# Optimization experiments

Hardware: AMD Instinct MI355X
Metric: run time of the kernel (lower is better)

## Reference

```python
import jax, jax.numpy as jnp
import numpy as np

EPS = 1e-5
NUM_HEADS = 16


def activation_quant(x):
    # 8-bit activation quant with straight-through estimator
    scale = 127.0 / jnp.clip(jnp.max(jnp.abs(x), axis=-1, keepdims=True), 1e-5, None)
    y = jnp.clip(jnp.round(x * scale), -128.0, 127.0) / scale
    return x + jax.lax.stop_gradient(y - x)


def weight_quant(w):
    # ternary {-1,0,1} weight quant with STE
    scale = 1.0 / jnp.clip(jnp.mean(jnp.abs(w)), 1e-5, None)
    wq = jnp.clip(jnp.round(w * scale), -1.0, 1.0) / scale
    return w + jax.lax.stop_gradient(wq - w)


def bitlinear(x, w):
    # F.layer_norm(x, x.shape[1:]): normalize over ALL dims except batch, no affine
    axes = tuple(range(1, x.ndim))
    mu = jnp.mean(x, axis=axes, keepdims=True)
    var = jnp.var(x, axis=axes, keepdims=True)
    xn = (x - mu) * jax.lax.rsqrt(var + EPS)
    return jnp.einsum('bnd,od->bno', activation_quant(xn), weight_quant(w))


def layer_norm(x, gamma, beta):
    mu = jnp.mean(x, axis=-1, keepdims=True)
    var = jnp.var(x, axis=-1, keepdims=True)
    return (x - mu) * jax.lax.rsqrt(var + EPS) * gamma + beta


def setup_inputs() -> dict:
    key = jax.random.key(0)
    k0, k1, k2 = jax.random.split(key, 3)
    B, N, D = 2, 2048, 1024
    return {
        't': jnp.zeros((1,), jnp.float32),
        'x': jax.random.normal(k0, (B, N, D), jnp.float32),
        'w_qkv': jax.random.normal(k1, (3 * D, D), jnp.float32) * 0.02,
        'w_out': jax.random.normal(k2, (D, D), jnp.float32) * 0.02,
        'gamma': jnp.ones((D,), jnp.float32),
        'beta': jnp.zeros((D,), jnp.float32),
    }


def reference(t, x, w_qkv, w_out, gamma, beta):
    B, N, D = x.shape
    H = NUM_HEADS
    hd = D // H
    scale = hd ** -0.5
    h = layer_norm(x, gamma, beta)                     # [B,N,D]
    qkv = bitlinear(h, w_qkv).reshape(B, N, 3, H, hd)   # [B,N,3,H,hd]
    qkv = jnp.transpose(qkv, (2, 0, 3, 1, 4))           # [3,B,H,N,hd]
    q, k, v = qkv[0], qkv[1], qkv[2]
    attn = jax.nn.softmax(jnp.einsum('bhnd,bhmd->bhnm', q, k) * scale, axis=-1)
    out = jnp.einsum('bhnm,bhmd->bhnd', attn, v)        # [B,H,N,hd]
    out = jnp.transpose(out, (0, 2, 1, 3)).reshape(B, N, D)
    return bitlinear(out, w_out)
```

## Files before the change

### kernel.cpp

```cpp
#include <hip/hip_runtime.h>
#include <hip/hip_bf16.h>
#include <hip/hip_fp16.h>
#include <math.h>

typedef __hip_bfloat16 bf16;
typedef int   i32x4 __attribute__((ext_vector_type(4)));
typedef float f32x4 __attribute__((ext_vector_type(4)));
typedef short bfx8  __attribute__((ext_vector_type(8)));

#define EPSV 1e-5f
#define NROWS 4096
#define DIM   1024
#define NSEQ  2048

__device__ __forceinline__ float ldv(const void* p, size_t i, int dt){
  if (dt == 0) return ((const float*)p)[i];
  if (dt == 1) return __bfloat162float(((const bf16*)p)[i]);
  return __half2float(((const __half*)p)[i]);
}

__device__ __forceinline__ void detect(const void* c0, const void* c1,
                                       int& dt, const void*& g, const void*& bta){
  unsigned u0 = *(const unsigned*)c0;
  int gfirst = (u0 != 0u) ? 1 : 0;
  g   = gfirst ? c0 : c1;
  bta = gfirst ? c1 : c0;
  unsigned short g0 = *(const unsigned short*)g;
  dt = (g0 == 0x3F80) ? 1 : ((g0 == 0x3C00) ? 2 : 0);
}

__device__ __forceinline__ float blk_sum(float v, float* sm){
  #pragma unroll
  for (int o = 32; o > 0; o >>= 1) v += __shfl_xor(v, o, 64);
  __syncthreads();
  if ((threadIdx.x & 63) == 0) sm[threadIdx.x >> 6] = v;
  __syncthreads();
  return sm[0] + sm[1] + sm[2] + sm[3];
}
__device__ __forceinline__ double blk_sum_d(double v, double* sm){
  #pragma unroll
  for (int o = 32; o > 0; o >>= 1) v += __shfl_xor(v, o, 64);
  __syncthreads();
  if ((threadIdx.x & 63) == 0) sm[threadIdx.x >> 6] = v;
  __syncthreads();
  return sm[0] + sm[1] + sm[2] + sm[3];
}
__device__ __forceinline__ float blk_max(float v, float* sm){
  #pragma unroll
  for (int o = 32; o > 0; o >>= 1) v = fmaxf(v, __shfl_xor(v, o, 64));
  __syncthreads();
  if ((threadIdx.x & 63) == 0) sm[threadIdx.x >> 6] = v;
  __syncthreads();
  return fmaxf(fmaxf(sm[0], sm[1]), fmaxf(sm[2], sm[3]));
}

__global__ __launch_bounds__(256) void ln_rows(const void* __restrict__ x,
                                               const void* __restrict__ c0,
                                               const void* __restrict__ c1,
                                               float* __restrict__ h,
                                               double* __restrict__ lnp){
  __shared__ float sm[4];
  __shared__ double smd[4];
  int dt; const void *g, *bta;
  detect(c0, c1, dt, g, bta);
  int row = blockIdx.x;
  int tid = threadIdx.x;
  float v[4]; float s = 0.f;
  float gmv[4], btv[4];
  if (dt == 0){
    float4 v4 = ((const float4*)x)[(size_t)row*256 + tid];
    v[0]=v4.x; v[1]=v4.y; v[2]=v4.z; v[3]=v4.w;
    float4 gm4 = ((const float4*)g)[tid];
    float4 bt4 = ((const float4*)bta)[tid];
    gmv[0]=gm4.x; gmv[1]=gm4.y; gmv[2]=gm4.z; gmv[3]=gm4.w;
    btv[0]=bt4.x; btv[1]=bt4.y; btv[2]=bt4.z; btv[3]=bt4.w;
  } else {
    size_t base = (size_t)row * DIM;
    #pragma unroll
    for (int i = 0; i < 4; ++i){
      v[i]   = ldv(x, base + 4*tid + i, dt);
      gmv[i] = ldv(g, 4*tid + i, dt);
      btv[i] = ldv(bta, 4*tid + i, dt);
    }
  }
  #pragma unroll
  for (int i = 0; i < 4; ++i) s += v[i];
  s = blk_sum(s, sm);
  float mu = s * (1.f/1024.f);
  float d2 = 0.f;
  #pragma unroll
  for (int i = 0; i < 4; ++i){ float d = v[i] - mu; d2 += d*d; }
  d2 = blk_sum(d2, sm);
  float rs = rsqrtf(d2 * (1.f/1024.f) + EPSV);
  float hv[4];
  #pragma unroll
  for (int i = 0; i < 4; ++i) hv[i] = (v[i]-mu)*rs*gmv[i] + btv[i];
  ((float4*)h)[(size_t)row*256 + tid] = make_float4(hv[0],hv[1],hv[2],hv[3]);
  double hs = 0.0, hq = 0.0;
  #pragma unroll
  for (int i = 0; i < 4; ++i){ hs += (double)hv[i]; hq += (double)hv[i]*(double)hv[i]; }
  hs = blk_sum_d(hs, smd);
  hq = blk_sum_d(hq, smd);
  if (tid == 0){ lnp[2*row] = hs; lnp[2*row + 1] = hq; }
}

__global__ __launch_bounds__(256) void abs_reduce_both(const void* __restrict__ wq,
                                                       const void* __restrict__ wo,
                                                       double* __restrict__ awp1,
                                                       double* __restrict__ awp2,
                                                       const void* __restrict__ c0,
                                                       const void* __restrict__ c1){
  __shared__ double smd[4];
  int dt; const void *g, *bta;
  detect(c0, c1, dt, g, bta);
  int blk = blockIdx.x;
  const void* w; int n; int nblk; int bi; double* part;
  if (blk < 512){ w = wq; n = 3*DIM*DIM; nblk = 512; bi = blk;      part = awp1; }
  else          { w = wo; n = DIM*DIM;   nblk = 128; bi = blk - 512; part = awp2; }
  double s = 0.0;
  if (dt == 0){
    const float4* w4 = (const float4*)w;
    int n4 = n >> 2;
    for (int i = bi*256 + threadIdx.x; i < n4; i += nblk*256){
      float4 v = w4[i];
      s += (double)(fabsf(v.x) + fabsf(v.y)) + (double)(fabsf(v.z) + fabsf(v.w));
    }
  } else {
    for (int i = bi*256 + threadIdx.x; i < n; i += nblk*256)
      s += (double)fabsf(ldv(w, i, dt));
  }
  s = blk_sum_d(s, smd);
  if (threadIdx.x == 0) part[bi] = s;
}

__global__ __launch_bounds__(256) void finalize1(float* acc,
                                                 const double* __restrict__ lnp,
                                                 const double* __restrict__ awp1,
                                                 const double* __restrict__ awp2){
  __shared__ double smd[4];
  int tid = threadIdx.x;
  double s0=0, q0=0, s1=0, q1=0, a1=0, a2=0;
  for (int i = tid; i < 2048; i += 256){
    s0 += lnp[2*i];          q0 += lnp[2*i + 1];
    s1 += lnp[2*(i+2048)];   q1 += lnp[2*(i+2048) + 1];
  }
  for (int i = tid; i < 512; i += 256) a1 += awp1[i];
  if (tid < 128) a2 = awp2[tid];
  s0 = blk_sum_d(s0, smd);  q0 = blk_sum_d(q0, smd);
  s1 = blk_sum_d(s1, smd);  q1 = blk_sum_d(q1, smd);
  a1 = blk_sum_d(a1, smd);  a2 = blk_sum_d(a2, smd);
  if (tid == 0){
    const double cnt = 2097152.0;
    double mu0 = s0/cnt, var0 = q0/cnt - mu0*mu0;
    double mu1 = s1/cnt, var1 = q1/cnt - mu1*mu1;
    acc[16] = (float)mu0; acc[17] = (float)(1.0 / sqrt(var0 + 1e-5));
    acc[18] = (float)mu1; acc[19] = (float)(1.0 / sqrt(var1 + 1e-5));
    acc[20] = (float)(1.0 / fmax(a1 / (3.0*1024.0*1024.0), 1e-5));
    acc[21] = (float)(1.0 / fmax(a2 / (1024.0*1024.0), 1e-5));
  }
}

__global__ __launch_bounds__(256) void finalize2(float* acc,
                                                 const double* __restrict__ atp){
  __shared__ double smd[4];
  int tid = threadIdx.x;
  double s0=0, q0=0, s1=0, q1=0;
  for (int i = tid; i < 512; i += 256){
    s0 += atp[2*i];          q0 += atp[2*i + 1];
    s1 += atp[2*(i+512)];    q1 += atp[2*(i+512) + 1];
  }
  s0 = blk_sum_d(s0, smd);  q0 = blk_sum_d(q0, smd);
  s1 = blk_sum_d(s1, smd);  q1 = blk_sum_d(q1, smd);
  if (tid == 0){
    const double cnt = 2097152.0;
    double mu0 = s0/cnt, var0 = q0/cnt - mu0*mu0;
    double mu1 = s1/cnt, var1 = q1/cnt - mu1*mu1;
    acc[22] = (float)mu0; acc[23] = (float)(1.0 / sqrt(var0 + 1e-5));
    acc[24] = (float)mu1; acc[25] = (float)(1.0 / sqrt(var1 + 1e-5));
  }
}

__global__ __launch_bounds__(256) void act_quant_i8(const float* __restrict__ buf,
                                                    signed char* __restrict__ qout,
                                                    float* __restrict__ rscale,
                                                    const float* __restrict__ acc,
                                                    int statOff){
  __shared__ float sm[4];
  int row = blockIdx.x;
  int b = row >> 11;
  float mu = acc[statOff + 2*b], rs = acc[statOff + 2*b + 1];
  int tid = threadIdx.x;
  float4 v4 = ((const float4*)buf)[(size_t)row*256 + tid];
  float v[4] = {(v4.x-mu)*rs, (v4.y-mu)*rs, (v4.z-mu)*rs, (v4.w-mu)*rs};
  float am = fmaxf(fmaxf(fabsf(v[0]), fabsf(v[1])), fmaxf(fabsf(v[2]), fabsf(v[3])));
  am = blk_max(am, sm);
  am = fmaxf(am, 1e-5f);
  float s127 = 127.f / am;
  unsigned pk = 0;
  #pragma unroll
  for (int i = 0; i < 4; ++i){
    float q = rintf(v[i] * s127);
    q = fminf(fmaxf(q, -128.f), 127.f);
    pk |= ((unsigned)(unsigned char)(signed char)q) << (8*i);
  }
  ((unsigned*)qout)[(size_t)row*256 + tid] = pk;
  if (tid == 0) rscale[row] = am * (1.f/127.f);
}

__global__ __launch_bounds__(256) void w_quant_both(const void* __restrict__ wqv,
                                                    const void* __restrict__ wov,
                                                    signed char* __restrict__ wqk,
                                                    signed char* __restrict__ wqo,
                                                    const float* __restrict__ acc,
                                                    const void* __restrict__ c0,
                                                    const void* __restrict__ c1){
  int dt; const void *g, *bta;
  detect(c0, c1, dt, g, bta);
  const int NQ4 = 786432;
  const int NT4 = 1048576;
  float s1 = acc[20], s2 = acc[21];
  if (dt == 0){
    for (int i = blockIdx.x*256 + threadIdx.x; i < NT4; i += gridDim.x*256){
      int inq = (i < NQ4);
      const float4* src = inq ? (const float4*)wqv : (const float4*)wov;
      unsigned* dst = inq ? (unsigned*)wqk : (unsigned*)wqo;
      int idx = inq ? i : (i - NQ4);
      float scale = inq ? s1 : s2;
      float4 v = src[idx];
      float vv[4] = {v.x, v.y, v.z, v.w};
      unsigned pk = 0;
      #pragma unroll
      for (int j = 0; j < 4; ++j){
        float q = rintf(vv[j] * scale);
        q = fminf(fmaxf(q, -1.f), 1.f);
        pk |= ((unsigned)(unsigned char)(signed char)q) << (8*j);
      }
      dst[idx] = pk;
    }
  } else {
    const int NQ = 3*DIM*DIM, NT = 4*DIM*DIM;
    for (int i = blockIdx.x*256 + threadIdx.x; i < NT; i += gridDim.x*256){
      int inq = (i < NQ);
      int idx = inq ? i : (i - NQ);
      float scale = inq ? s1 : s2;
      float q = rintf(ldv(inq ? wqv : wov, idx, dt) * scale);
      q = fminf(fmaxf(q, -1.f), 1.f);
      (inq ? wqk : wqo)[idx] = (signed char)q;
    }
  }
}

__global__ __launch_bounds__(256) void gemm_i8(const signed char* __restrict__ A,
                                               const signed char* __restrict__ W,
                                               const float* __restrict__ rscale,
                                               const float* __restrict__ acc, int sidx,
                                               float* __restrict__ Cf,
                                               bf16* __restrict__ Cb,
                                               int ldc, int writeBf, float q_prescale){
  __shared__ __attribute__((aligned(16))) signed char Asl[128][80];
  __shared__ __attribute__((aligned(16))) signed char Bsl[128][80];
  int tid = threadIdx.x, lane = tid & 63, w = tid >> 6;
  int wr = w >> 1, wc = w & 1;

  int nwgx = gridDim.x;
  int flat = blockIdx.y * nwgx + blockIdx.x;
  int nwg  = nwgx * gridDim.y;
  int cpx  = nwg >> 3;
  int swz  = (flat & 7) * cpx + (flat >> 3);
  int r0 = (swz / nwgx) * 128, o0 = (swz % nwgx) * 128;

  i32x4 zz = {0,0,0,0};
  i32x4 accv[4][4];
  #pragma unroll
  for (int m = 0; m < 4; ++m)
    #pragma unroll
    for (int n = 0; n < 4; ++n) accv[m][n] = zz;

  int sr0 = tid >> 2, sr1 = sr0 + 64;
  int sc  = (tid & 3) * 16;

  i32x4 a0, a1, b0, b1;
  a0 = *(const i32x4*)(A + (size_t)(r0 + sr0)*1024 + sc);
  a1 = *(const i32x4*)(A + (size_t)(r0 + sr1)*1024 + sc);
  b0 = *(const i32x4*)(W + (size_t)(o0 + sr0)*1024 + sc);
  b1 = *(const i32x4*)(W + (size_t)(o0 + sr1)*1024 + sc);

  for (int k0 = 0; k0 < 1024; k0 += 64){
    __syncthreads();
    *(i32x4*)&Asl[sr0][sc] = a0;
    *(i32x4*)&Asl[sr1][sc] = a1;
    *(i32x4*)&Bsl[sr0][sc] = b0;
    *(i32x4*)&Bsl[sr1][sc] = b1;
    __syncthreads();
    if (k0 + 64 < 1024){
      int kn = k0 + 64;
      a0 = *(const i32x4*)(A + (size_t)(r0 + sr0)*1024 + kn + sc);
      a1 = *(const i32x4*)(A + (size_t)(r0 + sr1)*1024 + kn + sc);
      b0 = *(const i32x4*)(W + (size_t)(o0 + sr0)*1024 + kn + sc);
      b1 = *(const i32x4*)(W + (size_t)(o0 + sr1)*1024 + kn + sc);
    }
    i32x4 af[4], bfr[4];
    #pragma unroll
    for (int m = 0; m < 4; ++m)
      af[m] = *(const i32x4*)&Asl[wr*64 + m*16 + (lane & 15)][(lane >> 4) * 16];
    #pragma unroll
    for (int n = 0; n < 4; ++n)
      bfr[n] = *(const i32x4*)&Bsl[wc*64 + n*16 + (lane & 15)][(lane >> 4) * 16];
    __builtin_amdgcn_s_setprio(1);
    #pragma unroll
    for (int m = 0; m < 4; ++m)
      #pragma unroll
      for (int n = 0; n < 4; ++n)
        accv[m][n] = __builtin_amdgcn_mfma_i32_16x16x64_i8(af[m], bfr[n], accv[m][n], 0, 0, 0);
    __builtin_amdgcn_s_setprio(0);
  }

  float wsc = acc[sidx];
  float cs = (o0 < 1024) ? q_prescale : 1.0f;
  float rf[4][4];
  #pragma unroll
  for (int m = 0; m < 4; ++m)
    #pragma unroll
    for (int r = 0; r < 4; ++r)
      rf[m][r] = rscale[r0 + wr*64 + m*16 + ((lane >> 4) << 2) + r] / wsc * cs;

  #pragma unroll
  for (int m = 0; m < 4; ++m)
    #pragma unroll
    for (int n = 0; n < 4; ++n)
      #pragma unroll
      for (int r = 0; r < 4; ++r){
        float val = (float)accv[m][n][r] * rf[m][r];
        size_t row = (size_t)(r0 + wr*64 + m*16 + ((lane >> 4) << 2) + r);
        int col = o0 + wc*64 + n*16 + (lane & 15);
        if (writeBf) Cb[row * ldc + col] = __float2bfloat16(val);
        else         Cf[row * ldc + col] = val;
      }
}

__global__ __launch_bounds__(256) void attn_mfma(const bf16* __restrict__ qkv,
                                                 float* __restrict__ out,
                                                 double* __restrict__ atp){
  __shared__ __attribute__((aligned(16))) unsigned short K_lds[64][64];
  __shared__ __attribute__((aligned(16))) unsigned short Vt_lds[64][64];
  __shared__ __attribute__((aligned(16))) unsigned short P_lds[4][16][64];
  __shared__ double smd[4];

  int tid = threadIdx.x, lane = tid & 63, w = tid >> 6;
  int l15 = lane & 15, g = lane >> 4;
  int h7 = l15 & 7;

  int flat = blockIdx.y * 32 + blockIdx.x;
  int slot = flat & 7, idx = flat >> 3;
  int bh = slot * 4 + (idx >> 5);
  int qx = idx & 31;
  int b = bh >> 4, h = bh & 15;
  int n0 = qx * 64;
  const unsigned short* qg = (const unsigned short*)qkv;

  char* kB = (char*)K_lds;
  char* vB = (char*)Vt_lds;
  char* pB = (char*)P_lds + w*2048;

  bfx8 qf[2];
  #pragma unroll
  for (int s = 0; s < 2; ++s){
    int qrow = b*NSEQ + n0 + w*16 + l15;
    qf[s] = *(const bfx8*)(qg + (size_t)qrow*3072 + h*64 + g*8 + s*32);
  }

  float m_run = -INFINITY, l_run = 0.f;
  f32x4 zf = {0.f, 0.f, 0.f, 0.f};
  f32x4 acco[4];
  #pragma unroll
  for (int n = 0; n < 4; ++n) acco[n] = zf;

  int krow = lane;
  int r2 = tid & 31, dwin = tid >> 5;
  int lh7 = lane & 7;

  bfx8 kc0, kc1, vv0, vv1;
  auto LOADT = [&](int kt){
    size_t kvb = (size_t)(b*NSEQ + kt*64);
    kc0 = *(const bfx8*)(qg + (kvb + krow)*3072 + 1024 + h*64 + w*8);
    kc1 = *(const bfx8*)(qg + (kvb + krow)*3072 + 1024 + h*64 + (w + 4)*8);
    vv0 = *(const bfx8*)(qg + (kvb + 2*r2    )*3072 + 2048 + h*64 + dwin*8);
    vv1 = *(const bfx8*)(qg + (kvb + 2*r2 + 1)*3072 + 2048 + h*64 + dwin*8);
  };
  LOADT(0);

  for (int kt = 0; kt < NSEQ/64; ++kt){
    __syncthreads();
    *(bfx8*)(kB + krow*128 + (((w    ) ^ lh7) << 4)) = kc0;
    *(bfx8*)(kB + krow*128 + (((w + 4) ^ lh7) << 4)) = kc1;
    #pragma unroll
    for (int u = 0; u < 8; ++u){
      unsigned word = (unsigned)(unsigned short)vv0[u] |
                      ((unsigned)(unsigned short)vv1[u] << 16);
      *(unsigned*)(vB + (dwin*8 + u)*128 + ((4*r2) ^ (u << 4))) = word;
    }
    __syncthreads();
    if (kt + 1 < NSEQ/64) LOADT(kt + 1);

    f32x4 sacc[4];
    #pragma unroll
    for (int f = 0; f < 4; ++f) sacc[f] = zf;
    #pragma unroll
    for (int f = 0; f < 4; ++f){
      bfx8 kb0 = *(const bfx8*)(kB + (f*16 + l15)*128 + (((g    ) ^ h7) << 4));
      bfx8 kb1 = *(const bfx8*)(kB + (f*16 + l15)*128 + (((g + 4) ^ h7) << 4));
      __builtin_amdgcn_s_setprio(1);
      sacc[f] = __builtin_amdgcn_mfma_f32_16x16x32_bf16(kb0, qf[0], sacc[f], 0, 0, 0);
      sacc[f] = __builtin_amdgcn_mfma_f32_16x16x32_bf16(kb1, qf[1], sacc[f], 0, 0, 0);
      __builtin_amdgcn_s_setprio(0);
    }

    float pm = sacc[0][0];
    #pragma unroll
    for (int f = 0; f < 4; ++f)
      #pragma unroll
      for (int r = 0; r < 4; ++r) pm = fmaxf(pm, sacc[f][r]);
    pm = fmaxf(pm, __shfl_xor(pm, 16, 64));
    pm = fmaxf(pm, __shfl_xor(pm, 32, 64));
    if (__any(pm > m_run + 8.f)){
      float mnew = fmaxf(m_run, pm);
      float corr = __expf(m_run - mnew);
      m_run = mnew;
      l_run *= corr;
      float ca[4];
      #pragma unroll
      for (int r = 0; r < 4; ++r) ca[r] = __shfl(corr, 4*g + r, 64);
      #pragma unroll
      for (int n = 0; n < 4; ++n)
        #pragma unroll
        for (int r = 0; r < 4; ++r) acco[n][r] *= ca[r];
    }
    float p[4][4]; float ts = 0.f;
    #pragma unroll
    for (int f = 0; f < 4; ++f)
      #pragma unroll
      for (int r = 0; r < 4; ++r){
        p[f][r] = __expf(sacc[f][r] - m_run);
        ts += p[f][r];
      }
    ts += __shfl_xor(ts, 16, 64);
    ts += __shfl_xor(ts, 32, 64);
    l_run += ts;

    #pragma unroll
    for (int f = 0; f < 4; ++f)
      #pragma unroll
      for (int rp = 0; rp < 2; ++rp){
        unsigned pk;
        asm("v_cvt_pk_bf16_f32 %0, %1, %2" : "=v"(pk)
            : "v"(p[f][2*rp]), "v"(p[f][2*rp+1]));
        *(unsigned*)(pB + l15*128 + ((32*f + 8*g + 4*rp) ^ (h7 << 4))) = pk;
      }

    bfx8 pa[2];
    #pragma unroll
    for (int s = 0; s < 2; ++s)
      pa[s] = *(const bfx8*)(pB + l15*128 + (((g + 4*s) ^ h7) << 4));
    #pragma unroll
    for (int n = 0; n < 4; ++n){
      bfx8 vb0 = *(const bfx8*)(vB + (n*16 + l15)*128 + (((g    ) ^ h7) << 4));
      bfx8 vb1 = *(const bfx8*)(vB + (n*16 + l15)*128 + (((g + 4) ^ h7) << 4));
      __builtin_amdgcn_s_setprio(1);
      acco[n] = __builtin_amdgcn_mfma_f32_16x16x32_bf16(pa[0], vb0, acco[n], 0, 0, 0);
      acco[n] = __builtin_amdgcn_mfma_f32_16x16x32_bf16(pa[1], vb1, acco[n], 0, 0, 0);
      __builtin_amdgcn_s_setprio(0);
    }
  }

  float il = 1.f / l_run;
  float ila[4];
  #pragma unroll
  for (int r = 0; r < 4; ++r) ila[r] = __shfl(il, 4*g + r, 64);
  double ssum = 0.0, ssq = 0.0;
  #pragma unroll
  for (int n = 0; n < 4; ++n)
    #pragma unroll
    for (int r = 0; r < 4; ++r){
      float o = acco[n][r] * ila[r];
      int orow = b*NSEQ + n0 + w*16 + 4*g + r;
      out[(size_t)orow * DIM + h*64 + n*16 + l15] = o;
      ssum += (double)o; ssq += (double)o * (double)o;
    }
  ssum = blk_sum_d(ssum, smd);
  ssq  = blk_sum_d(ssq, smd);
  if (tid == 0){
    int bflat = bh * 32 + qx;
    atp[2*bflat] = ssum; atp[2*bflat + 1] = ssq;
  }
}

extern "C" void kernel_launch(void* const* d_in, const int* in_sizes, int n_in,
                              void* d_out, int out_size, void* d_ws, size_t ws_size,
                              hipStream_t stream) {
  int ix = -1, iwq = -1, iwo = -1, ig0 = -1, ig1 = -1;
  for (int i = 0; i < n_in; ++i){
    int s = in_sizes[i];
    if      (s == 4194304) ix  = i;
    else if (s == 3145728) iwq = i;
    else if (s == 1048576) iwo = i;
    else if (s == 1024){ if (ig0 < 0) ig0 = i; else ig1 = i; }
  }
  if (ix < 0 || iwq < 0 || iwo < 0 || ig0 < 0 || ig1 < 0){ ix=1; iwq=2; iwo=3; ig0=4; ig1=5; }
  const void* x     = d_in[ix];
  const void* w_qkv = d_in[iwq];
  const void* w_out = d_in[iwo];
  const void* g0    = d_in[ig0];
  const void* g1    = d_in[ig1];

  char* ws = (char*)d_ws;
  float*  acc     = (float*)ws;
  float*  rscale1 = (float*)(ws + 12288);
  float*  rscale2 = (float*)(ws + 28672);
  double* lnp     = (double*)(ws + 65536);
  double* awp1    = (double*)(ws + 131072);
  double* awp2    = (double*)(ws + 135168);
  double* atp     = (double*)(ws + 139264);
  float*        h      = (float*)      (ws + (1u<<20));
  signed char*  h_i8   = (signed char*)(ws + (17u<<20));
  signed char*  wqk_i8 = (signed char*)(ws + (21u<<20));
  signed char*  wqo_i8 = (signed char*)(ws + (24u<<20));
  bf16*         qkvb   = (bf16*)       (ws + (25u<<20));
  signed char*  a2_i8  = (signed char*)(ws + (49u<<20));
  float*        aout   = h;

  ln_rows<<<NROWS, 256, 0, stream>>>(x, g0, g1, h, lnp);
  abs_reduce_both<<<640, 256, 0, stream>>>(w_qkv, w_out, awp1, awp2, g0, g1);
  finalize1<<<1, 256, 0, stream>>>(acc, lnp, awp1, awp2);
  act_quant_i8<<<NROWS, 256, 0, stream>>>(h, h_i8, rscale1, acc, 16);
  w_quant_both<<<1024, 256, 0, stream>>>(w_qkv, w_out, wqk_i8, wqo_i8, acc, g0, g1);
  gemm_i8<<<dim3(24, 32), 256, 0, stream>>>(h_i8, wqk_i8, rscale1, acc, 20,
                                            nullptr, qkvb, 3072, 1, 0.125f);
  attn_mfma<<<dim3(32, 32), 256, 0, stream>>>(qkvb, aout, atp);
  finalize2<<<1, 256, 0, stream>>>(acc, atp);
  act_quant_i8<<<NROWS, 256, 0, stream>>>(aout, a2_i8, rscale2, acc, 22);
  gemm_i8<<<dim3(8, 32), 256, 0, stream>>>(a2_i8, wqo_i8, rscale2, acc, 21,
                                           (float*)d_out, nullptr, 1024, 0, 1.0f);
}
```

Measured before the change: 154.2 us.

## Switch attention kernel to 32x32x16 MFMA with register-resident P via permlane32 swap

Rewrites the flash-attention kernel to use 32x32x16 bf16 MFMA tiles with two waves of 32 query rows each (128 threads) instead of four waves of 16 rows. The softmax probabilities are packed to bf16 and rearranged between lane halves with v_permlane32_swap, so they feed the PV MFMA directly from registers and the P round-trip through LDS is gone. The aim is fewer MFMA issues and fewer LDS accesses per tile. In exchange each thread loads more K/V per tile, register pressure per thread rises, and blocks are smaller, which may change occupancy and latency hiding.

```diff
diff --git a/kernel.cpp b/kernel.cpp
--- a/kernel.cpp
+++ b/kernel.cpp
@@ -4,9 +4,10 @@
 #include <math.h>
 
 typedef __hip_bfloat16 bf16;
-typedef int   i32x4 __attribute__((ext_vector_type(4)));
-typedef float f32x4 __attribute__((ext_vector_type(4)));
-typedef short bfx8  __attribute__((ext_vector_type(8)));
+typedef int   i32x4  __attribute__((ext_vector_type(4)));
+typedef float f32x4  __attribute__((ext_vector_type(4)));
+typedef float f32x16 __attribute__((ext_vector_type(16)));
+typedef short bfx8   __attribute__((ext_vector_type(8)));
 
 #define EPSV 1e-5f
 #define NROWS 4096
@@ -338,17 +339,15 @@
       }
 }
 
-__global__ __launch_bounds__(256) void attn_mfma(const bf16* __restrict__ qkv,
+__global__ __launch_bounds__(128) void attn_mfma(const bf16* __restrict__ qkv,
                                                  float* __restrict__ out,
                                                  double* __restrict__ atp){
   __shared__ __attribute__((aligned(16))) unsigned short K_lds[64][64];
   __shared__ __attribute__((aligned(16))) unsigned short Vt_lds[64][64];
-  __shared__ __attribute__((aligned(16))) unsigned short P_lds[4][16][64];
-  __shared__ double smd[4];
+  __shared__ double smd[2];
 
   int tid = threadIdx.x, lane = tid & 63, w = tid >> 6;
-  int l15 = lane & 15, g = lane >> 4;
-  int h7 = l15 & 7;
+  int l31 = lane & 31, hi = lane >> 5;
 
   int flat = blockIdx.y * 32 + blockIdx.x;
   int slot = flat & 7, idx = flat >> 3;
@@ -360,137 +359,149 @@
 
   char* kB = (char*)K_lds;
   char* vB = (char*)Vt_lds;
-  char* pB = (char*)P_lds + w*2048;
-
-  bfx8 qf[2];
-  #pragma unroll
-  for (int s = 0; s < 2; ++s){
-    int qrow = b*NSEQ + n0 + w*16 + l15;
-    qf[s] = *(const bfx8*)(qg + (size_t)qrow*3072 + h*64 + g*8 + s*32);
-  }
+
+  int qrow = b*NSEQ + n0 + w*32 + l31;
+  bfx8 qf[4];
+  #pragma unroll
+  for (int kk = 0; kk < 4; ++kk)
+    qf[kk] = *(const bfx8*)(qg + (size_t)qrow*3072 + h*64 + kk*16 + hi*8);
 
   float m_run = -INFINITY, l_run = 0.f;
-  f32x4 zf = {0.f, 0.f, 0.f, 0.f};
-  f32x4 acco[4];
-  #pragma unroll
-  for (int n = 0; n < 4; ++n) acco[n] = zf;
-
-  int krow = lane;
-  int r2 = tid & 31, dwin = tid >> 5;
-  int lh7 = lane & 7;
-
-  bfx8 kc0, kc1, vv0, vv1;
+  f32x16 acco[2];
+  #pragma unroll
+  for (int n = 0; n < 2; ++n)
+    #pragma unroll
+    for (int r = 0; r < 16; ++r) acco[n][r] = 0.f;
+
+  int krow = tid & 63;
+  int r2 = tid & 31, dw = tid >> 5;
+  int k7 = krow & 7;
+
+  bfx8 kc[4], vv[4];
   auto LOADT = [&](int kt){
     size_t kvb = (size_t)(b*NSEQ + kt*64);
-    kc0 = *(const bfx8*)(qg + (kvb + krow)*3072 + 1024 + h*64 + w*8);
-    kc1 = *(const bfx8*)(qg + (kvb + krow)*3072 + 1024 + h*64 + (w + 4)*8);
-    vv0 = *(const bfx8*)(qg + (kvb + 2*r2    )*3072 + 2048 + h*64 + dwin*8);
-    vv1 = *(const bfx8*)(qg + (kvb + 2*r2 + 1)*3072 + 2048 + h*64 + dwin*8);
+    #pragma unroll
+    for (int j = 0; j < 4; ++j)
+      kc[j] = *(const bfx8*)(qg + (kvb + krow)*3072 + 1024 + h*64 + (w + 2*j)*8);
+    vv[0] = *(const bfx8*)(qg + (kvb + 2*r2    )*3072 + 2048 + h*64 + dw*8);
+    vv[1] = *(const bfx8*)(qg + (kvb + 2*r2 + 1)*3072 + 2048 + h*64 + dw*8);
+    vv[2] = *(const bfx8*)(qg + (kvb + 2*r2    )*3072 + 2048 + h*64 + (dw+4)*8);
+    vv[3] = *(const bfx8*)(qg + (kvb + 2*r2 + 1)*3072 + 2048 + h*64 + (dw+4)*8);
   };
   LOADT(0);
 
   for (int kt = 0; kt < NSEQ/64; ++kt){
     __syncthreads();
-    *(bfx8*)(kB + krow*128 + (((w    ) ^ lh7) << 4)) = kc0;
-    *(bfx8*)(kB + krow*128 + (((w + 4) ^ lh7) << 4)) = kc1;
+    #pragma unroll
+    for (int j = 0; j < 4; ++j)
+      *(bfx8*)(kB + krow*128 + (((w + 2*j) ^ k7) << 4)) = kc[j];
     #pragma unroll
     for (int u = 0; u < 8; ++u){
-      unsigned word = (unsigned)(unsigned short)vv0[u] |
-                      ((unsigned)(unsigned short)vv1[u] << 16);
-      *(unsigned*)(vB + (dwin*8 + u)*128 + ((4*r2) ^ (u << 4))) = word;
+      unsigned w0 = (unsigned)(unsigned short)vv[0][u] |
+                    ((unsigned)(unsigned short)vv[1][u] << 16);
+      unsigned w1 = (unsigned)(unsigned short)vv[2][u] |
+                    ((unsigned)(unsigned short)vv[3][u] << 16);
+      *(unsigned*)(vB + (dw*8 + u)*128     + ((4*r2) ^ (u << 4))) = w0;
+      *(unsigned*)(vB + ((dw+4)*8 + u)*128 + ((4*r2) ^ (u << 4))) = w1;
     }
     __syncthreads();
     if (kt + 1 < NSEQ/64) LOADT(kt + 1);
 
-    f32x4 sacc[4];
-    #pragma unroll
-    for (int f = 0; f < 4; ++f) sacc[f] = zf;
-    #pragma unroll
-    for (int f = 0; f < 4; ++f){
-      bfx8 kb0 = *(const bfx8*)(kB + (f*16 + l15)*128 + (((g    ) ^ h7) << 4));
-      bfx8 kb1 = *(const bfx8*)(kB + (f*16 + l15)*128 + (((g + 4) ^ h7) << 4));
+    f32x16 s0, s1;
+    #pragma unroll
+    for (int r = 0; r < 16; ++r){ s0[r] = 0.f; s1[r] = 0.f; }
+    int q7 = l31 & 7;
+    #pragma unroll
+    for (int kk = 0; kk < 4; ++kk){
+      bfx8 kb0 = *(const bfx8*)(kB + l31*128        + (((2*kk + hi) ^ q7) << 4));
+      bfx8 kb1 = *(const bfx8*)(kB + (32 + l31)*128 + (((2*kk + hi) ^ q7) << 4));
       __builtin_amdgcn_s_setprio(1);
-      sacc[f] = __builtin_amdgcn_mfma_f32_16x16x32_bf16(kb0, qf[0], sacc[f], 0, 0, 0);
-      sacc[f] = __builtin_amdgcn_mfma_f32_16x16x32_bf16(kb1, qf[1], sacc[f], 0, 0, 0);
+      s0 = __builtin_amdgcn_mfma_f32_32x32x16_bf16(kb0, qf[kk], s0, 0, 0, 0);
+      s1 = __builtin_amdgcn_mfma_f32_32x32x16_bf16(kb1, qf[kk], s1, 0, 0, 0);
       __builtin_amdgcn_s_setprio(0);
     }
 
-    float pm = sacc[0][0];
-    #pragma unroll
-    for (int f = 0; f < 4; ++f)
-      #pragma unroll
-      for (int r = 0; r < 4; ++r) pm = fmaxf(pm, sacc[f][r]);
-    pm = fmaxf(pm, __shfl_xor(pm, 16, 64));
+    float pm = s0[0];
+    #pragma unroll
+    for (int r = 1; r < 16; ++r) pm = fmaxf(pm, s0[r]);
+    #pragma unroll
+    for (int r = 0; r < 16; ++r) pm = fmaxf(pm, s1[r]);
     pm = fmaxf(pm, __shfl_xor(pm, 32, 64));
     if (__any(pm > m_run + 8.f)){
       float mnew = fmaxf(m_run, pm);
       float corr = __expf(m_run - mnew);
       m_run = mnew;
       l_run *= corr;
-      float ca[4];
       #pragma unroll
-      for (int r = 0; r < 4; ++r) ca[r] = __shfl(corr, 4*g + r, 64);
-      #pragma unroll
-      for (int n = 0; n < 4; ++n)
-        #pragma unroll
-        for (int r = 0; r < 4; ++r) acco[n][r] *= ca[r];
-    }
-    float p[4][4]; float ts = 0.f;
-    #pragma unroll
-    for (int f = 0; f < 4; ++f)
-      #pragma unroll
-      for (int r = 0; r < 4; ++r){
-        p[f][r] = __expf(sacc[f][r] - m_run);
-        ts += p[f][r];
+      for (int r = 0; r < 16; ++r){
+        float ca = __shfl(corr, (r & 3) + 8*(r >> 2) + 4*hi, 64);
+        acco[0][r] *= ca; acco[1][r] *= ca;
       }
-    ts += __shfl_xor(ts, 16, 64);
+    }
+    float ts = 0.f;
+    #pragma unroll
+    for (int r = 0; r < 16; ++r){
+      s0[r] = __expf(s0[r] - m_run); ts += s0[r];
+      s1[r] = __expf(s1[r] - m_run); ts += s1[r];
+    }
     ts += __shfl_xor(ts, 32, 64);
     l_run += ts;
 
     #pragma unroll
-    for (int f = 0; f < 4; ++f)
+    for (int kvb = 0; kvb < 2; ++kvb){
+      const f32x16& s = kvb ? s1 : s0;
       #pragma unroll
-      for (int rp = 0; rp < 2; ++rp){
-        unsigned pk;
-        asm("v_cvt_pk_bf16_f32 %0, %1, %2" : "=v"(pk)
-            : "v"(p[f][2*rp]), "v"(p[f][2*rp+1]));
-        *(unsigned*)(pB + l15*128 + ((32*f + 8*g + 4*rp) ^ (h7 << 4))) = pk;
+      for (int kk2 = 0; kk2 < 2; ++kk2){
+        int bse = kk2 * 8;
+        unsigned wa, wb2, wc, wd;
+        asm("v_cvt_pk_bf16_f32 %0, %1, %2" : "=v"(wa)  : "v"(s[bse+0]), "v"(s[bse+1]));
+        asm("v_cvt_pk_bf16_f32 %0, %1, %2" : "=v"(wb2) : "v"(s[bse+4]), "v"(s[bse+5]));
+        asm("v_cvt_pk_bf16_f32 %0, %1, %2" : "=v"(wc)  : "v"(s[bse+2]), "v"(s[bse+3]));
+        asm("v_cvt_pk_bf16_f32 %0, %1, %2" : "=v"(wd)  : "v"(s[bse+6]), "v"(s[bse+7]));
+        asm("v_permlane32_swap_b32 %0, %1" : "+v"(wa), "+v"(wb2));
+        asm("v_permlane32_swap_b32 %0, %1" : "+v"(wc), "+v"(wd));
+        unsigned pw[4] = {wa, wc, wb2, wd};
+        bfx8 pa = *(bfx8*)pw;
+        #pragma unroll
+        for (int n = 0; n < 2; ++n){
+          bfx8 vb = *(const bfx8*)(vB + (n*32 + l31)*128 +
+                                   (((kvb*4 + kk2*2 + hi) ^ q7) << 4));
+          __builtin_amdgcn_s_setprio(1);
+          acco[n] = __builtin_amdgcn_mfma_f32_32x32x16_bf16(pa, vb, acco[n], 0, 0, 0);
+          __builtin_amdgcn_s_setprio(0);
+        }
       }
-
-    bfx8 pa[2];
-    #pragma unroll
-    for (int s = 0; s < 2; ++s)
-      pa[s] = *(const bfx8*)(pB + l15*128 + (((g + 4*s) ^ h7) << 4));
-    #pragma unroll
-    for (int n = 0; n < 4; ++n){
-      bfx8 vb0 = *(const bfx8*)(vB + (n*16 + l15)*128 + (((g    ) ^ h7) << 4));
-      bfx8 vb1 = *(const bfx8*)(vB + (n*16 + l15)*128 + (((g + 4) ^ h7) << 4));
-      __builtin_amdgcn_s_setprio(1);
-      acco[n] = __builtin_amdgcn_mfma_f32_16x16x32_bf16(pa[0], vb0, acco[n], 0, 0, 0);
-      acco[n] = __builtin_amdgcn_mfma_f32_16x16x32_bf16(pa[1], vb1, acco[n], 0, 0, 0);
-      __builtin_amdgcn_s_setprio(0);
     }
   }
 
   float il = 1.f / l_run;
-  float ila[4];
-  #pragma unroll
-  for (int r = 0; r < 4; ++r) ila[r] = __shfl(il, 4*g + r, 64);
+  float ila[16];
+  #pragma unroll
+  for (int r = 0; r < 16; ++r)
+    ila[r] = __shfl(il, (r & 3) + 8*(r >> 2) + 4*hi, 64);
   double ssum = 0.0, ssq = 0.0;
   #pragma unroll
-  for (int n = 0; n < 4; ++n)
-    #pragma unroll
-    for (int r = 0; r < 4; ++r){
+  for (int n = 0; n < 2; ++n)
+    #pragma unroll
+    for (int r = 0; r < 16; ++r){
       float o = acco[n][r] * ila[r];
-      int orow = b*NSEQ + n0 + w*16 + 4*g + r;
-      out[(size_t)orow * DIM + h*64 + n*16 + l15] = o;
+      int orow = b*NSEQ + n0 + w*32 + (r & 3) + 8*(r >> 2) + 4*hi;
+      out[(size_t)orow * DIM + h*64 + n*32 + l31] = o;
       ssum += (double)o; ssq += (double)o * (double)o;
     }
-  ssum = blk_sum_d(ssum, smd);
-  ssq  = blk_sum_d(ssq, smd);
+  #pragma unroll
+  for (int o = 32; o > 0; o >>= 1){ ssum += __shfl_xor(ssum, o, 64); ssq += __shfl_xor(ssq, o, 64); }
+  __syncthreads();
+  if (lane == 0){ smd[w] = ssum; }
+  __syncthreads();
+  double tsum = smd[0] + smd[1];
+  __syncthreads();
+  if (lane == 0){ smd[w] = ssq; }
+  __syncthreads();
+  double tsq = smd[0] + smd[1];
   if (tid == 0){
     int bflat = bh * 32 + qx;
-    atp[2*bflat] = ssum; atp[2*bflat + 1] = ssq;
+    atp[2*bflat] = tsum; atp[2*bflat + 1] = tsq;
   }
 }
 
@@ -535,7 +546,7 @@
   w_quant_both<<<1024, 256, 0, stream>>>(w_qkv, w_out, wqk_i8, wqo_i8, acc, g0, g1);
   gemm_i8<<<dim3(24, 32), 256, 0, stream>>>(h_i8, wqk_i8, rscale1, acc, 20,
                                             nullptr, qkvb, 3072, 1, 0.125f);
-  attn_mfma<<<dim3(32, 32), 256, 0, stream>>>(qkvb, aout, atp);
+  attn_mfma<<<dim3(32, 32), 128, 0, stream>>>(qkvb, aout, atp);
   finalize2<<<1, 256, 0, stream>>>(acc, atp);
   act_quant_i8<<<NROWS, 256, 0, stream>>>(aout, a2_i8, rscale2, acc, 22);
   gemm_i8<<<dim3(8, 32), 256, 0, stream>>>(a2_i8, wqo_i8, rscale2, acc, 21,
```

Measured after the change: 150.1 us. -2.7%, faster.
